# Performance work log

Hardware: AMD Instinct MI355X
Metric: run time of the kernel (lower is better)

Reference implementation:

```python
import jax, jax.numpy as jnp
import numpy as np

# geomloss SamplesLoss defaults: loss='sinkhorn', p=2, blur=0.05, scaling=0.5,
# reach=None (balanced -> dampening lambda = 1), diameter=3, debias=False.
P = 2
DIAMETER = 3.0
BLUR = 0.05
SCALING = 0.5
MARGIN = 0.1
GAMMA = 10.0
# geomloss epsilon_schedule(p, diameter, blur, scaling)
EPS_LIST = [DIAMETER ** P] \
    + [float(np.exp(e)) for e in np.arange(P * np.log(DIAMETER), P * np.log(BLUR), P * np.log(SCALING))] \
    + [BLUR ** P]
NEG_INF_LOGW = -100000.0  # geomloss log_weights() sentinel for zero weights


def similarity_cost(xa, xb, gamma=GAMMA):
    # F.normalize(x, dim=-1): x / max(||x||, 1e-12)
    xa = xa / jnp.clip(jnp.linalg.norm(xa, axis=-1, keepdims=True), 1e-12)
    xb = xb / jnp.clip(jnp.linalg.norm(xb, axis=-1, keepdims=True), 1e-12)
    sim = jnp.exp(jnp.einsum('bnd,bmd->bnm', xa, xb) * gamma)  # (B, N, M)
    sim_c = sim.sum(axis=1, keepdims=True)  # column sums (B, 1, M)
    sim_r = sim.sum(axis=2, keepdims=True)  # row sums    (B, N, 1)
    return 1.0 - sim / (sim_c + sim_r - sim)


def softmin(eps, C, h):
    # geomloss softmin_tensorized: -eps * logsumexp_j(h_j - C_ij/eps)
    # C: (B, N, M), h: (B_or_1, M) -> (B, N)
    return -eps * jax.nn.logsumexp(h[:, None, :] - C / eps, axis=2)


def sinkhorn_ot(alpha, a_log, beta, b_log, f1, f2):
    # geomloss sinkhorn_tensorized with debias=False, balanced OT.
    C_xy = similarity_cost(f1, jax.lax.stop_gradient(f2))  # cost(x, y.detach())
    C_yx = similarity_cost(f2, jax.lax.stop_gradient(f1))  # cost(y, x.detach())
    C_xy_sg = jax.lax.stop_gradient(C_xy)
    C_yx_sg = jax.lax.stop_gradient(C_yx)

    eps = EPS_LIST[0]
    g_ab = softmin(eps, C_yx_sg, a_log)  # dual potential on y
    f_ba = softmin(eps, C_xy_sg, b_log)  # dual potential on x
    for eps in EPS_LIST:
        # symmetric (averaged) Sinkhorn updates, no grad (geomloss runs under no_grad)
        ft = softmin(eps, C_xy_sg, b_log + g_ab / eps)
        gt = softmin(eps, C_yx_sg, a_log + f_ba / eps)
        f_ba, g_ab = 0.5 * (f_ba + ft), 0.5 * (g_ab + gt)

    # last extrapolation: only differentiable step (detached dual inputs)
    eps = EPS_LIST[-1]
    f_ba_new = softmin(eps, C_xy, jax.lax.stop_gradient(b_log + g_ab / eps))
    g_ab_new = softmin(eps, C_yx, jax.lax.stop_gradient(a_log + f_ba / eps))

    # sinkhorn_cost (debias=False): <alpha, f_ba> + <beta, g_ab>
    return (alpha * f_ba_new).sum(axis=1) + (beta * g_ab_new).sum(axis=1)  # (B,)


def setup_inputs() -> dict:
    key = jax.random.key(0)
    k1, k2, k3, k4, k5 = jax.random.split(key, 5)
    B, N, N1, M1, D = 16, 512, 384, 384, 256
    return {
        'x1': jax.random.normal(k1, (B, N, D), dtype=jnp.float32),
        'x2': jax.random.normal(k2, (B, N, D), dtype=jnp.float32),
        'x3': jax.random.normal(k3, (B, N1, D), dtype=jnp.float32),
        'x4': jax.random.normal(k4, (B, M1, D), dtype=jnp.float32),
        'dist': jax.random.normal(k5, (16,), dtype=jnp.float32),  # stored but unused
    }


def reference(x1, x2, x3, x4, dist):
    B, N, _ = x1.shape
    N1 = x3.shape[1]
    M1 = x4.shape[1]
    dt = x1.dtype
    # marginals: ones over real points, zeros over padding points
    alpha = jnp.concatenate([jnp.ones((1, N), dt), jnp.zeros((1, N1), dt)], axis=1)
    beta = jnp.concatenate([jnp.ones((1, N), dt), jnp.zeros((1, M1), dt)], axis=1)
    a_log = jnp.concatenate([jnp.zeros((1, N), dt), jnp.full((1, N1), NEG_INF_LOGW, dt)], axis=1)
    b_log = jnp.concatenate([jnp.zeros((1, N), dt), jnp.full((1, M1), NEG_INF_LOGW, dt)], axis=1)

    f1 = jnp.concatenate([x1, x3], axis=1)  # (B, N+N1, D)
    f2 = jnp.concatenate([x2, x4], axis=1)  # (B, N+M1, D)

    ot_loss = sinkhorn_ot(alpha, a_log, beta, b_log, f1, f2)  # (B,)
    scon_cost = jnp.mean(ot_loss)[None]  # sum(ot_loss)/B, shape (1,)

    hinge = jax.nn.relu(MARGIN - jnp.einsum('bnd,bmd->bnm', x3, x4)).sum()
    hinge_cost = hinge[None]  # shape (1,)

    # original returns {'hinge_cost': ..., 'scon_cost': ...}; pack as (2,) array
    return jnp.concatenate([hinge_cost, scon_cost])
```

## Files before the change

kernel.cpp:

```cpp
#include <hip/hip_runtime.h>
#include <cstddef>
#include <cstdint>

#define BATCH 16
#define NFULL 896
#define NREAL 512
#define NPAD  384
#define DIM   256

typedef short bf16x8 __attribute__((ext_vector_type(8)));
typedef short s16x4  __attribute__((ext_vector_type(4)));
typedef float f32x4  __attribute__((ext_vector_type(4)));
typedef int   int4v  __attribute__((ext_vector_type(4)));

static __device__ inline short f2bf(float v) {
    unsigned u = __float_as_uint(v);
    unsigned r = (u + 0x7FFFu + ((u >> 16) & 1u)) >> 16;
    return (short)r;
}
static __device__ inline float bf2f(short s) {
    return __uint_as_float(((unsigned)(unsigned short)s) << 16);
}

__global__ __launch_bounds__(256) void norm_cvt_kernel(
    const float* __restrict__ x1, const float* __restrict__ x3,
    const float* __restrict__ x2, const float* __restrict__ x4,
    short* __restrict__ A1s, short* __restrict__ B2s,
    float* __restrict__ invn1, float* __restrict__ invn2,
    float* __restrict__ n1, float* __restrict__ n2,
    float* __restrict__ zero_base, float* __restrict__ out)
{
    const int t = threadIdx.x;
    const int gid = blockIdx.x * 256 + t;
    if (gid < 2 * BATCH * NFULL) zero_base[gid] = 0.f;
    if (gid < 2) out[gid] = 0.f;

    const int w = t >> 6, lane = t & 63;
    const int rg = blockIdx.x * 4 + w;
    const int side = rg >= BATCH * NFULL;
    const int rem  = rg - (side ? BATCH * NFULL : 0);
    const int b = rem / NFULL, row = rem % NFULL;
    const float* src;
    if (!side) src = (row < NREAL) ? x1 + ((size_t)b * NREAL + row) * DIM
                                   : x3 + ((size_t)b * NPAD + (row - NREAL)) * DIM;
    else       src = (row < NREAL) ? x2 + ((size_t)b * NREAL + row) * DIM
                                   : x4 + ((size_t)b * NPAD + (row - NREAL)) * DIM;
    const f32x4 v = ((const f32x4*)src)[lane];
    float ss = v[0]*v[0] + v[1]*v[1] + v[2]*v[2] + v[3]*v[3];
    #pragma unroll
    for (int m = 1; m < 64; m <<= 1) ss += __shfl_xor(ss, m);
    const float nrm = sqrtf(ss);
    const float inv = 1.0f / fmaxf(nrm, 1e-12f);
    if (lane == 0) {
        (side ? invn2 : invn1)[b * NFULL + row] = inv;
        (side ? n2 : n1)[b * NFULL + row] = nrm;
    }
    s16x4 hi, lo;
    #pragma unroll
    for (int c = 0; c < 4; ++c) {
        const float val = v[c] * inv;
        hi[c] = f2bf(val);
        lo[c] = f2bf(val - bf2f(hi[c]));
    }
    short* dst = (side ? B2s : A1s) + ((size_t)b * NFULL + row) * 512;
    *(s16x4*)(dst + lane * 4) = hi;
    *(s16x4*)(dst + 256 + lane * 4) = lo;
}

__global__ __launch_bounds__(256) void gram_mfma_kernel(
    const short* __restrict__ A1s, const short* __restrict__ B2s,
    const float* __restrict__ n1, const float* __restrict__ n2,
    float* __restrict__ S, float* __restrict__ rowsum, float* __restrict__ colsum,
    float* __restrict__ out_hinge)
{
    const int flat = blockIdx.x;
    const int id = (flat & 7) * 98 + (flat >> 3);
    const int b  = id / 49;
    const int r49 = id % 49;
    const int by = r49 / 7, bx = r49 % 7;
    const int i0 = by * 128;
    const int j0 = bx * 128;
    __shared__ __align__(16) short As[128][72];
    __shared__ __align__(16) short Bs[128][72];
    const int t = threadIdx.x;
    const int wid = t >> 6, lane = t & 63;
    const int wr = wid >> 1, wc = wid & 1;
    const int lr = lane & 15, lg = lane >> 4;
    f32x4 acc[4][4] = {};

    const short* gA = A1s + ((size_t)b * NFULL + i0) * 512;
    const short* gB = B2s + ((size_t)b * NFULL + j0) * 512;

    for (int step = 0; step < 12; ++step) {
        const int kb   = step * 64;
        const int koff = kb & 255;
        const int aoff = (((kb >> 8) == 1) ? 256 : 0) + koff;
        const int boff = (((kb >> 8) == 2) ? 256 : 0) + koff;
        __syncthreads();
        #pragma unroll
        for (int p = 0; p < 4; ++p) {
            const int s = p * 256 + t;
            const int row = s >> 3, c = s & 7;
            *(int4v*)((char*)&As[0][0] + row * 144 + c * 16) =
                *(const int4v*)(gA + (size_t)row * 512 + aoff + c * 8);
            *(int4v*)((char*)&Bs[0][0] + row * 144 + c * 16) =
                *(const int4v*)(gB + (size_t)row * 512 + boff + c * 8);
        }
        __syncthreads();
        #pragma unroll
        for (int kk = 0; kk < 64; kk += 32) {
            bf16x8 af[4], bg[4];
            #pragma unroll
            for (int m = 0; m < 4; ++m)
                af[m] = *(const bf16x8*)((const char*)&As[0][0]
                         + (wr * 64 + m * 16 + lr) * 144 + kk * 2 + lg * 16);
            #pragma unroll
            for (int n = 0; n < 4; ++n)
                bg[n] = *(const bf16x8*)((const char*)&Bs[0][0]
                         + (wc * 64 + n * 16 + lr) * 144 + kk * 2 + lg * 16);
            #pragma unroll
            for (int m = 0; m < 4; ++m)
                #pragma unroll
                for (int n = 0; n < 4; ++n)
                    acc[m][n] = __builtin_amdgcn_mfma_f32_16x16x32_bf16(
                        af[m], bg[n], acc[m][n], 0, 0, 0);
        }
    }

    const bool storeS = (by < 4) && (bx < 4);
    const bool hingeB = (by >= 4) && (bx >= 4);
    float rp[4][4] = {};
    float cp[4] = {};
    float hp = 0.f;
    #pragma unroll
    for (int m = 0; m < 4; ++m) {
        const int row0 = i0 + wr * 64 + m * 16 + lg * 4;
        float n1v[4] = {0.f, 0.f, 0.f, 0.f};
        if (hingeB) {
            #pragma unroll
            for (int r = 0; r < 4; ++r) n1v[r] = n1[b * NFULL + row0 + r];
        }
        #pragma unroll
        for (int n = 0; n < 4; ++n) {
            const int col = j0 + wc * 64 + n * 16 + lr;
            const f32x4 f = acc[m][n];
            float cn = 0.f;
            float sv[4];
            #pragma unroll
            for (int r = 0; r < 4; ++r) {
                sv[r] = __expf(10.f * f[r]);
                rp[m][r] += sv[r];
                cn += sv[r];
            }
            cp[n] += cn;
            if (storeS) {
                #pragma unroll
                for (int r = 0; r < 4; ++r)
                    S[((size_t)b * NREAL + row0 + r) * NREAL + col] = sv[r];
            }
            if (hingeB) {
                const float nn2 = n2[b * NFULL + col];
                #pragma unroll
                for (int r = 0; r < 4; ++r)
                    hp += fmaxf(0.1f - f[r] * n1v[r] * nn2, 0.f);
            }
        }
    }
    #pragma unroll
    for (int m = 0; m < 4; ++m)
        #pragma unroll
        for (int r = 0; r < 4; ++r) {
            float v = rp[m][r];
            v += __shfl_xor(v, 1); v += __shfl_xor(v, 2);
            v += __shfl_xor(v, 4); v += __shfl_xor(v, 8);
            if (lr == 0)
                atomicAdd(&rowsum[b * NFULL + i0 + wr * 64 + m * 16 + lg * 4 + r], v);
        }
    #pragma unroll
    for (int n = 0; n < 4; ++n) {
        float v = cp[n];
        v += __shfl_xor(v, 16); v += __shfl_xor(v, 32);
        if (lg == 0)
            atomicAdd(&colsum[b * NFULL + j0 + wc * 64 + n * 16 + lr], v);
    }
    if (hingeB) {
        #pragma unroll
        for (int m = 1; m < 64; m <<= 1) hp += __shfl_xor(hp, m);
        if (lane == 0) atomicAdd(out_hinge, hp);
    }
}

__global__ __launch_bounds__(256) void norm_kernel(
    const float* __restrict__ x1, const float* __restrict__ x3,
    const float* __restrict__ x2, const float* __restrict__ x4,
    float* __restrict__ invn1, float* __restrict__ invn2)
{
    const int w = threadIdx.x >> 6, lane = threadIdx.x & 63;
    const int rg = blockIdx.x * 4 + w;
    const int side = rg / (BATCH * NFULL);
    const int rem  = rg - side * (BATCH * NFULL);
    const int b = rem / NFULL, r = rem % NFULL;
    const float* src;
    if (side == 0)
        src = (r < NREAL) ? x1 + ((size_t)b * NREAL + r) * DIM
                          : x3 + ((size_t)b * NPAD + (r - NREAL)) * DIM;
    else
        src = (r < NREAL) ? x2 + ((size_t)b * NREAL + r) * DIM
                          : x4 + ((size_t)b * NPAD + (r - NREAL)) * DIM;
    float4 v = ((const float4*)src)[lane];
    float ss = v.x*v.x + v.y*v.y + v.z*v.z + v.w*v.w;
    #pragma unroll
    for (int m = 1; m < 64; m <<= 1) ss += __shfl_xor(ss, m);
    if (lane == 0)
        (side == 0 ? invn1 : invn2)[b * NFULL + r] = 1.0f / fmaxf(sqrtf(ss), 1e-12f);
}

__global__ __launch_bounds__(256) void gram_kernel(
    const float* __restrict__ x1, const float* __restrict__ x3,
    const float* __restrict__ x2, const float* __restrict__ x4,
    const float* __restrict__ invn1, const float* __restrict__ invn2,
    float* __restrict__ S, float* __restrict__ rowsum, float* __restrict__ colsum)
{
    const int b  = blockIdx.z;
    const int i0 = blockIdx.y * 64;
    const int j0 = blockIdx.x * 64;
    __shared__ float As[64][68];
    __shared__ float Bs[64][68];
    __shared__ float rsh[64], csh[64];
    const int t = threadIdx.x;
    const int tx = t & 15, ty = t >> 4;
    if (t < 64) { rsh[t] = 0.f; csh[t] = 0.f; }
    float acc[4][4] = {};
    const int lk = t & 63, r4 = t >> 6;
    for (int kc = 0; kc < DIM; kc += 64) {
        __syncthreads();
        #pragma unroll
        for (int rr = 0; rr < 64; rr += 4) {
            const int r = rr + r4;
            const int gi = i0 + r;
            const float* pa = (gi < NREAL) ? x1 + ((size_t)b * NREAL + gi) * DIM
                                           : x3 + ((size_t)b * NPAD + (gi - NREAL)) * DIM;
            As[r][lk] = pa[kc + lk] * invn1[b * NFULL + gi];
            const int gj = j0 + r;
            const float* pb = (gj < NREAL) ? x2 + ((size_t)b * NREAL + gj) * DIM
                                           : x4 + ((size_t)b * NPAD + (gj - NREAL)) * DIM;
            Bs[r][lk] = pb[kc + lk] * invn2[b * NFULL + gj];
        }
        __syncthreads();
        #pragma unroll
        for (int k = 0; k < 64; k += 4) {
            float4 av[4], bv[4];
            #pragma unroll
            for (int u = 0; u < 4; ++u) av[u] = *(const float4*)&As[ty + 16*u][k];
            #pragma unroll
            for (int u = 0; u < 4; ++u) bv[u] = *(const float4*)&Bs[tx + 16*u][k];
            #pragma unroll
            for (int u = 0; u < 4; ++u)
                #pragma unroll
                for (int v = 0; v < 4; ++v) {
                    acc[u][v] += av[u].x * bv[v].x;
                    acc[u][v] += av[u].y * bv[v].y;
                    acc[u][v] += av[u].z * bv[v].z;
                    acc[u][v] += av[u].w * bv[v].w;
                }
        }
    }
    float rpart[4] = {}, cpart[4] = {};
    const bool store = (i0 < NREAL) && (j0 < NREAL);
    #pragma unroll
    for (int u = 0; u < 4; ++u)
        #pragma unroll
        for (int v = 0; v < 4; ++v) {
            const float s = __expf(10.0f * acc[u][v]);
            rpart[u] += s;
            cpart[v] += s;
            if (store) {
                const int i = i0 + ty + 16*u, j = j0 + tx + 16*v;
                S[((size_t)b * NREAL + i) * NREAL + j] = s;
            }
        }
    #pragma unroll
    for (int u = 0; u < 4; ++u) atomicAdd(&rsh[ty + 16*u], rpart[u]);
    #pragma unroll
    for (int v = 0; v < 4; ++v) atomicAdd(&csh[tx + 16*v], cpart[v]);
    __syncthreads();
    if (t < 64) {
        atomicAdd(&rowsum[b * NFULL + i0 + t], rsh[t]);
        atomicAdd(&colsum[b * NFULL + j0 + t], csh[t]);
    }
}

__global__ __launch_bounds__(256) void hinge_kernel(
    const float* __restrict__ x3, const float* __restrict__ x4, float* __restrict__ out)
{
    const int b  = blockIdx.z;
    const int i0 = blockIdx.y * 64;
    const int j0 = blockIdx.x * 64;
    __shared__ float As[64][68];
    __shared__ float Bs[64][68];
    const int t = threadIdx.x;
    const int tx = t & 15, ty = t >> 4;
    float acc[4][4] = {};
    const int lk = t & 63, r4 = t >> 6;
    for (int kc = 0; kc < DIM; kc += 64) {
        __syncthreads();
        #pragma unroll
        for (int rr = 0; rr < 64; rr += 4) {
            const int r = rr + r4;
            As[r][lk] = x3[((size_t)b * NPAD + i0 + r) * DIM + kc + lk];
            Bs[r][lk] = x4[((size_t)b * NPAD + j0 + r) * DIM + kc + lk];
        }
        __syncthreads();
        #pragma unroll
        for (int k = 0; k < 64; k += 4) {
            float4 av[4], bv[4];
            #pragma unroll
            for (int u = 0; u < 4; ++u) av[u] = *(const float4*)&As[ty + 16*u][k];
            #pragma unroll
            for (int u = 0; u < 4; ++u) bv[u] = *(const float4*)&Bs[tx + 16*u][k];
            #pragma unroll
            for (int u = 0; u < 4; ++u)
                #pragma unroll
                for (int v = 0; v < 4; ++v) {
                    acc[u][v] += av[u].x * bv[v].x;
                    acc[u][v] += av[u].y * bv[v].y;
                    acc[u][v] += av[u].z * bv[v].z;
                    acc[u][v] += av[u].w * bv[v].w;
                }
        }
    }
    float part = 0.f;
    #pragma unroll
    for (int u = 0; u < 4; ++u)
        #pragma unroll
        for (int v = 0; v < 4; ++v) part += fmaxf(0.1f - acc[u][v], 0.f);
    __shared__ float red[256];
    red[t] = part;
    __syncthreads();
    for (int s = 128; s > 0; s >>= 1) { if (t < s) red[t] += red[t + s]; __syncthreads(); }
    if (t == 0) atomicAdd(out, red[0]);
}

__global__ __launch_bounds__(256) void cost_kernel(
    float* __restrict__ C, float* __restrict__ CT,
    const float* __restrict__ rowsum, const float* __restrict__ colsum)
{
    const int b  = blockIdx.z;
    const int i0 = blockIdx.y * 64, j0 = blockIdx.x * 64;
    __shared__ float tile[64][65];
    const int t = threadIdx.x;
    const int lj = t & 63, r4 = t >> 6;
    #pragma unroll
    for (int rr = 0; rr < 64; rr += 4) {
        const int li = rr + r4;
        const size_t idx = ((size_t)b * NREAL + i0 + li) * NREAL + j0 + lj;
        const float s  = C[idx];
        const float rs = rowsum[b * NFULL + i0 + li];
        const float cs = colsum[b * NFULL + j0 + lj];
        const float c = 1.0f - s / (rs + cs - s);
        C[idx] = c;
        tile[li][lj] = c;
    }
    if (CT == nullptr) return;
    __syncthreads();
    #pragma unroll
    for (int rr = 0; rr < 4 * 16; rr += 4) {
        const int lc = rr + r4;
        CT[((size_t)b * NREAL + j0 + lc) * NREAL + i0 + lj] = tile[lj][lc];
    }
}

__global__ __launch_bounds__(256) void softmin_kernel(
    const float* __restrict__ C, const float* __restrict__ CT,
    const float* __restrict__ f_in, const float* __restrict__ g_in,
    float* __restrict__ f_out, float* __restrict__ g_out,
    float eps, int mode, float* __restrict__ out)
{
    const int w = threadIdx.x >> 6, lane = threadIdx.x & 63;
    const int rg = blockIdx.x * 4 + w;
    const int side = rg >= 2048;
    const int rem  = side ? rg - 2048 : rg;
    const int b  = rem >> 7;
    const int ib = (rem & 127) * 4;
    const float inv_eps = 1.0f / eps;
    const float* h_src = (side ? f_in : g_in) + b * NREAL;

    f32x4 h0 = {0.f, 0.f, 0.f, 0.f}, h1 = h0;
    if (mode != 0) {
        const f32x4* h4 = (const f32x4*)h_src;
        h0 = h4[lane] * inv_eps;
        h1 = h4[64 + lane] * inv_eps;
    }

    const float* Mb;
    size_t stride;
    if (!side)   { Mb = C  + ((size_t)(b * NREAL + ib)) * NREAL; stride = 1; }
    else if (CT) { Mb = CT + ((size_t)(b * NREAL + ib)) * NREAL; stride = 1; }
    else         { Mb = C + (size_t)b * NREAL * NREAL + ib;      stride = NREAL; }

    float res[4];
    float acc_res = 0.f;
    if (stride == 1) {
        f32x4 A0[4], A1[4];
        #pragma unroll
        for (int rr = 0; rr < 4; ++rr) {
            const f32x4* M4 = (const f32x4*)(Mb + (size_t)rr * NREAL);
            A0[rr] = M4[lane];
            A1[rr] = M4[64 + lane];
        }
        #pragma unroll
        for (int rr = 0; rr < 4; ++rr) {
            const f32x4 v0 = h0 - A0[rr] * inv_eps;
            const f32x4 v1 = h1 - A1[rr] * inv_eps;
            float mx = fmaxf(fmaxf(fmaxf(v0[0], v0[1]), fmaxf(v0[2], v0[3])),
                             fmaxf(fmaxf(v1[0], v1[1]), fmaxf(v1[2], v1[3])));
            #pragma unroll
            for (int off = 1; off < 64; off <<= 1) mx = fmaxf(mx, __shfl_xor(mx, off));
            float s = 0.f;
            #pragma unroll
            for (int c = 0; c < 4; ++c) s += __expf(v0[c] - mx);
            #pragma unroll
            for (int c = 0; c < 4; ++c) s += __expf(v1[c] - mx);
            #pragma unroll
            for (int off = 1; off < 64; off <<= 1) s += __shfl_xor(s, off);
            res[rr] = -eps * (mx + __logf(s));
            acc_res += res[rr];
        }
    } else {
        #pragma unroll
        for (int rr = 0; rr < 4; ++rr) {
            const float* M = Mb + rr;
            float v[8];
            #pragma unroll
            for (int q = 0; q < 8; ++q) {
                const float h = (q < 4) ? h0[q & 3] : h1[q & 3];
                v[q] = h - M[(size_t)((q & 3) + (q >> 2) * 256 + lane * 4) * NREAL
                             - (size_t)(lane * 4 + (q & 3) + (q >> 2) * 256) * 0] * inv_eps;
            }
            #pragma unroll
            for (int q = 0; q < 8; ++q) {
                const int j = (q >> 2) * 256 + lane * 4 + (q & 3);
                v[q] = ((q < 4) ? h0[q & 3] : h1[q & 3]) - M[(size_t)j * NREAL] * inv_eps;
            }
            float mx = v[0];
            #pragma unroll
            for (int q = 1; q < 8; ++q) mx = fmaxf(mx, v[q]);
            #pragma unroll
            for (int off = 1; off < 64; off <<= 1) mx = fmaxf(mx, __shfl_xor(mx, off));
            float s = 0.f;
            #pragma unroll
            for (int q = 0; q < 8; ++q) s += __expf(v[q] - mx);
            #pragma unroll
            for (int off = 1; off < 64; off <<= 1) s += __shfl_xor(s, off);
            res[rr] = -eps * (mx + __logf(s));
            acc_res += res[rr];
        }
    }

    if (mode == 2) {
        __shared__ float sred[4];
        if (lane == 0) sred[w] = acc_res;
        __syncthreads();
        if (threadIdx.x == 0)
            atomicAdd(out, (sred[0] + sred[1] + sred[2] + sred[3]) * (1.0f / BATCH));
    } else if (lane == 0) {
        float* st = (side ? g_out : f_out) + b * NREAL + ib;
        if (mode == 0) {
            *(f32x4*)st = f32x4{res[0], res[1], res[2], res[3]};
        } else {
            const f32x4 si = *(const f32x4*)((side ? g_in : f_in) + b * NREAL + ib);
            *(f32x4*)st = 0.5f * (si + f32x4{res[0], res[1], res[2], res[3]});
        }
    }
}

extern "C" void kernel_launch(void* const* d_in, const int* in_sizes, int n_in,
                              void* d_out, int out_size, void* d_ws, size_t ws_size,
                              hipStream_t stream)
{
    const float* x1 = (const float*)d_in[0];
    const float* x2 = (const float*)d_in[1];
    const float* x3 = (const float*)d_in[2];
    const float* x4 = (const float*)d_in[3];
    float* out = (float*)d_out;

    char* p = (char*)d_ws;
    const size_t CBYTES = (size_t)BATCH * NREAL * NREAL * 4;
    const size_t ABYTES = (size_t)BATCH * NFULL * 512 * 2;
    const size_t NB = (size_t)BATCH * NFULL * 4;
    const size_t PB = (size_t)BATCH * NREAL * 4;
    const size_t SMALLB = 6 * NB + 4 * PB;
    const bool mfma_ok = ws_size >= CBYTES + 2 * ABYTES + SMALLB;

    float* C = (float*)p; p += CBYTES;
    short* A1s = nullptr; short* B2s = nullptr;
    float* CT = nullptr;
    if (mfma_ok) {
        A1s = (short*)p; p += ABYTES;
        B2s = (short*)p; p += ABYTES;
        CT = (float*)A1s;
    }
    float* rowsum = (float*)p; p += NB;
    float* colsum = (float*)p; p += NB;
    float* invn1  = (float*)p; p += NB;
    float* invn2  = (float*)p; p += NB;
    float* n1     = (float*)p; p += NB;
    float* n2     = (float*)p; p += NB;
    float* fs     = (float*)p; p += 2 * PB;
    float* gs     = (float*)p; p += 2 * PB;
    if (!mfma_ok && ws_size >= (size_t)(p - (char*)d_ws) + CBYTES) {
        CT = (float*)p; p += CBYTES;
    }
    const int PS = BATCH * NREAL;

    if (mfma_ok) {
        norm_cvt_kernel<<<(2 * BATCH * NFULL) / 4, 256, 0, stream>>>(
            x1, x3, x2, x4, A1s, B2s, invn1, invn2, n1, n2, rowsum, out);
        gram_mfma_kernel<<<784, 256, 0, stream>>>(
            A1s, B2s, n1, n2, C, rowsum, colsum, out);
    } else {
        hipMemsetAsync(out, 0, 2 * sizeof(float), stream);
        hipMemsetAsync(rowsum, 0, 2 * NB, stream);
        norm_kernel<<<(2 * BATCH * NFULL) / 4, 256, 0, stream>>>(
            x1, x3, x2, x4, invn1, invn2);
        gram_kernel<<<dim3(14, 14, BATCH), 256, 0, stream>>>(
            x1, x3, x2, x4, invn1, invn2, C, rowsum, colsum);
        hinge_kernel<<<dim3(6, 6, BATCH), 256, 0, stream>>>(x3, x4, out);
    }
    cost_kernel<<<dim3(8, 8, BATCH), 256, 0, stream>>>(C, CT, rowsum, colsum);

    const int SMB = 1024;
    const float epsl[8] = {9.0f, 9.0f, 2.25f, 0.5625f, 0.140625f,
                           0.03515625f, 0.0087890625f, 0.0025f};

    softmin_kernel<<<SMB, 256, 0, stream>>>(C, CT, fs, gs, fs, gs, 9.0f, 0, out);
    int cur = 0;
    for (int k = 0; k < 8; ++k) {
        softmin_kernel<<<SMB, 256, 0, stream>>>(C, CT,
            fs + cur * PS, gs + cur * PS,
            fs + (1 - cur) * PS, gs + (1 - cur) * PS,
            epsl[k], 1, out);
        cur ^= 1;
    }
    softmin_kernel<<<SMB, 256, 0, stream>>>(C, CT,
        fs + cur * PS, gs + cur * PS, nullptr, nullptr,
        0.0025f, 2, out + 1);
}
```

Measured before the change: 200.8 us.

## Double-buffer gram tiles via direct global-to-LDS loads and XCD-aware block mapping

The gram MFMA kernel now stages operands with global_load_lds into double-buffered, XOR-swizzled shared tiles of 32-wide K slices, so the next slice's load overlaps the current MFMAs. This replaces register-staged copies and the full sync pair per step. Row and column sum atomics are skipped for padding tiles that are never used. The cost and softmin kernels remap block indices so each XCD handles two batches, keeping C rows in that XCD's L2. The risks are manual vmcnt counting, more barriers per K step, and a changed softmin register-prefetch pattern.

```diff
diff --git a/kernel.cpp b/kernel.cpp
--- a/kernel.cpp
+++ b/kernel.cpp
@@ -11,7 +11,6 @@
 typedef short bf16x8 __attribute__((ext_vector_type(8)));
 typedef short s16x4  __attribute__((ext_vector_type(4)));
 typedef float f32x4  __attribute__((ext_vector_type(4)));
-typedef int   int4v  __attribute__((ext_vector_type(4)));
 
 static __device__ inline short f2bf(float v) {
     unsigned u = __float_as_uint(v);
@@ -20,6 +19,15 @@
 }
 static __device__ inline float bf2f(short s) {
     return __uint_as_float(((unsigned)(unsigned short)s) << 16);
+}
+
+static __device__ __forceinline__ void gload_lds16(const void* g, size_t lds_byte_off,
+                                                   void* lds_base) {
+    __builtin_amdgcn_global_load_lds(
+        (const __attribute__((address_space(1))) unsigned int*)(size_t)g,
+        (__attribute__((address_space(3))) unsigned int*)(unsigned int)
+            ((size_t)lds_base + lds_byte_off),
+        16, 0, 0);
 }
 
 __global__ __launch_bounds__(256) void norm_cvt_kernel(
@@ -80,8 +88,8 @@
     const int by = r49 / 7, bx = r49 % 7;
     const int i0 = by * 128;
     const int j0 = bx * 128;
-    __shared__ __align__(16) short As[128][72];
-    __shared__ __align__(16) short Bs[128][72];
+    __shared__ __align__(16) short As[2][128][32];
+    __shared__ __align__(16) short Bs[2][128][32];
     const int t = threadIdx.x;
     const int wid = t >> 6, lane = t & 63;
     const int wr = wid >> 1, wc = wid & 1;
@@ -91,41 +99,64 @@
     const short* gA = A1s + ((size_t)b * NFULL + i0) * 512;
     const short* gB = B2s + ((size_t)b * NFULL + j0) * 512;
 
-    for (int step = 0; step < 12; ++step) {
-        const int kb   = step * 64;
-        const int koff = kb & 255;
-        const int aoff = (((kb >> 8) == 1) ? 256 : 0) + koff;
-        const int boff = (((kb >> 8) == 2) ? 256 : 0) + koff;
-        __syncthreads();
-        #pragma unroll
-        for (int p = 0; p < 4; ++p) {
-            const int s = p * 256 + t;
-            const int row = s >> 3, c = s & 7;
-            *(int4v*)((char*)&As[0][0] + row * 144 + c * 16) =
-                *(const int4v*)(gA + (size_t)row * 512 + aoff + c * 8);
-            *(int4v*)((char*)&Bs[0][0] + row * 144 + c * 16) =
-                *(const int4v*)(gB + (size_t)row * 512 + boff + c * 8);
-        }
-        __syncthreads();
-        #pragma unroll
-        for (int kk = 0; kk < 64; kk += 32) {
-            bf16x8 af[4], bg[4];
-            #pragma unroll
-            for (int m = 0; m < 4; ++m)
-                af[m] = *(const bf16x8*)((const char*)&As[0][0]
-                         + (wr * 64 + m * 16 + lr) * 144 + kk * 2 + lg * 16);
+    int srow[2], scl[2];
+    #pragma unroll
+    for (int p = 0; p < 2; ++p) {
+        const int s = p * 256 + t;
+        srow[p] = s >> 2;
+        scl[p] = (s & 3) ^ (srow[p] & 3);
+    }
+
+    #define GRAM_ISSUE(step, buf)                                              \
+        do {                                                                   \
+            const int kb_   = (step) * 32;                                     \
+            const int koff_ = kb_ & 255;                                       \
+            const int aoff_ = (((kb_ >> 8) == 1) ? 256 : 0) + koff_;           \
+            const int boff_ = (((kb_ >> 8) == 2) ? 256 : 0) + koff_;           \
+            _Pragma("unroll")                                                  \
+            for (int p = 0; p < 2; ++p)                                        \
+                gload_lds16(gA + (size_t)srow[p] * 512 + aoff_ + scl[p] * 8,   \
+                            (size_t)(p * 256 + wid * 64) * 16,                 \
+                            &As[buf][0][0]);                                   \
+            _Pragma("unroll")                                                  \
+            for (int p = 0; p < 2; ++p)                                        \
+                gload_lds16(gB + (size_t)srow[p] * 512 + boff_ + scl[p] * 8,   \
+                            (size_t)(p * 256 + wid * 64) * 16,                 \
+                            &Bs[buf][0][0]);                                   \
+        } while (0)
+
+    GRAM_ISSUE(0, 0);
+    for (int step = 0; step < 24; ++step) {
+        const int cur = step & 1;
+        if (step + 1 < 24) {
+            GRAM_ISSUE(step + 1, cur ^ 1);
+            asm volatile("s_waitcnt vmcnt(4)" ::: "memory");
+        } else {
+            asm volatile("s_waitcnt vmcnt(0)" ::: "memory");
+        }
+        __builtin_amdgcn_s_barrier();
+        bf16x8 af[4], bg[4];
+        #pragma unroll
+        for (int m = 0; m < 4; ++m) {
+            const int row = wr * 64 + m * 16 + lr;
+            af[m] = *(const bf16x8*)((const char*)&As[cur][0][0]
+                     + row * 64 + (((lg) ^ (row & 3)) << 4));
+        }
+        #pragma unroll
+        for (int n = 0; n < 4; ++n) {
+            const int row = wc * 64 + n * 16 + lr;
+            bg[n] = *(const bf16x8*)((const char*)&Bs[cur][0][0]
+                     + row * 64 + (((lg) ^ (row & 3)) << 4));
+        }
+        #pragma unroll
+        for (int m = 0; m < 4; ++m)
             #pragma unroll
             for (int n = 0; n < 4; ++n)
-                bg[n] = *(const bf16x8*)((const char*)&Bs[0][0]
-                         + (wc * 64 + n * 16 + lr) * 144 + kk * 2 + lg * 16);
-            #pragma unroll
-            for (int m = 0; m < 4; ++m)
-                #pragma unroll
-                for (int n = 0; n < 4; ++n)
-                    acc[m][n] = __builtin_amdgcn_mfma_f32_16x16x32_bf16(
-                        af[m], bg[n], acc[m][n], 0, 0, 0);
-        }
-    }
+                acc[m][n] = __builtin_amdgcn_mfma_f32_16x16x32_bf16(
+                    af[m], bg[n], acc[m][n], 0, 0, 0);
+        __builtin_amdgcn_s_barrier();
+    }
+    #undef GRAM_ISSUE
 
     const bool storeS = (by < 4) && (bx < 4);
     const bool hingeB = (by >= 4) && (bx >= 4);
@@ -166,27 +197,139 @@
             }
         }
     }
-    #pragma unroll
-    for (int m = 0; m < 4; ++m)
-        #pragma unroll
-        for (int r = 0; r < 4; ++r) {
-            float v = rp[m][r];
-            v += __shfl_xor(v, 1); v += __shfl_xor(v, 2);
-            v += __shfl_xor(v, 4); v += __shfl_xor(v, 8);
-            if (lr == 0)
-                atomicAdd(&rowsum[b * NFULL + i0 + wr * 64 + m * 16 + lg * 4 + r], v);
-        }
-    #pragma unroll
-    for (int n = 0; n < 4; ++n) {
-        float v = cp[n];
-        v += __shfl_xor(v, 16); v += __shfl_xor(v, 32);
-        if (lg == 0)
-            atomicAdd(&colsum[b * NFULL + j0 + wc * 64 + n * 16 + lr], v);
+    if (by < 4) {
+        #pragma unroll
+        for (int m = 0; m < 4; ++m)
+            #pragma unroll
+            for (int r = 0; r < 4; ++r) {
+                float v = rp[m][r];
+                v += __shfl_xor(v, 1); v += __shfl_xor(v, 2);
+                v += __shfl_xor(v, 4); v += __shfl_xor(v, 8);
+                if (lr == 0)
+                    atomicAdd(&rowsum[b * NFULL + i0 + wr * 64 + m * 16 + lg * 4 + r], v);
+            }
+    }
+    if (bx < 4) {
+        #pragma unroll
+        for (int n = 0; n < 4; ++n) {
+            float v = cp[n];
+            v += __shfl_xor(v, 16); v += __shfl_xor(v, 32);
+            if (lg == 0)
+                atomicAdd(&colsum[b * NFULL + j0 + wc * 64 + n * 16 + lr], v);
+        }
     }
     if (hingeB) {
         #pragma unroll
         for (int m = 1; m < 64; m <<= 1) hp += __shfl_xor(hp, m);
         if (lane == 0) atomicAdd(out_hinge, hp);
+    }
+}
+
+__global__ __launch_bounds__(256) void cost_kernel(
+    float* __restrict__ C, float* __restrict__ CT,
+    const float* __restrict__ rowsum, const float* __restrict__ colsum)
+{
+    const int blk = blockIdx.x;
+    const int xcd = blk & 7, q = blk >> 3;
+    const int b = 2 * xcd + (q >> 6);
+    const int t64 = q & 63;
+    const int i0 = (t64 >> 3) * 64, j0 = (t64 & 7) * 64;
+    __shared__ float tile[64][65];
+    const int t = threadIdx.x;
+    const int lj = t & 63, r4 = t >> 6;
+    #pragma unroll
+    for (int rr = 0; rr < 64; rr += 4) {
+        const int li = rr + r4;
+        const size_t idx = ((size_t)b * NREAL + i0 + li) * NREAL + j0 + lj;
+        const float s  = C[idx];
+        const float c = 1.0f - s / (rowsum[b * NFULL + i0 + li]
+                                    + colsum[b * NFULL + j0 + lj] - s);
+        C[idx] = c;
+        tile[li][lj] = c;
+    }
+    if (CT == nullptr) return;
+    __syncthreads();
+    #pragma unroll
+    for (int rr = 0; rr < 64; rr += 4) {
+        const int lc = rr + r4;
+        CT[((size_t)b * NREAL + j0 + lc) * NREAL + i0 + lj] = tile[lj][lc];
+    }
+}
+
+__global__ __launch_bounds__(256) void softmin_kernel(
+    const float* __restrict__ C, const float* __restrict__ CT,
+    const float* __restrict__ f_in, const float* __restrict__ g_in,
+    float* __restrict__ f_out, float* __restrict__ g_out,
+    float eps, int mode, float* __restrict__ out)
+{
+    const int w = threadIdx.x >> 6, lane = threadIdx.x & 63;
+    const int blk = blockIdx.x;
+    const int xcd = blk & 7, q = blk >> 3;
+    const int b = 2 * xcd + (q >> 6);
+    const int side = (q >> 5) & 1;
+    const int ib = ((q & 31) * 4 + w) * 4;
+    const float inv_eps = 1.0f / eps;
+    const float* h_src = (side ? f_in : g_in) + b * NREAL;
+
+    f32x4 h0 = {0.f, 0.f, 0.f, 0.f}, h1 = h0;
+    if (mode != 0) {
+        const f32x4* h4 = (const f32x4*)h_src;
+        h0 = h4[lane] * inv_eps;
+        h1 = h4[64 + lane] * inv_eps;
+    }
+    const float* Mb;
+    size_t stride;
+    if (!side)   { Mb = C  + ((size_t)(b * NREAL + ib)) * NREAL; stride = 1; }
+    else if (CT) { Mb = CT + ((size_t)(b * NREAL + ib)) * NREAL; stride = 1; }
+    else         { Mb = C + (size_t)b * NREAL * NREAL + ib;      stride = NREAL; }
+
+    float res[4];
+    float acc_res = 0.f;
+    #pragma unroll
+    for (int rr = 0; rr < 4; ++rr) {
+        float v[8];
+        if (stride == 1) {
+            const f32x4* M4 = (const f32x4*)(Mb + (size_t)rr * NREAL);
+            const f32x4 a0 = M4[lane], a1 = M4[64 + lane];
+            #pragma unroll
+            for (int c = 0; c < 4; ++c) { v[c] = h0[c] - a0[c] * inv_eps;
+                                          v[4+c] = h1[c] - a1[c] * inv_eps; }
+        } else {
+            const float* M = Mb + rr;
+            #pragma unroll
+            for (int qq = 0; qq < 8; ++qq) {
+                const int j = (qq >> 2) * 256 + lane * 4 + (qq & 3);
+                v[qq] = ((qq < 4) ? h0[qq & 3] : h1[qq & 3])
+                        - M[(size_t)j * NREAL] * inv_eps;
+            }
+        }
+        float mx = v[0];
+        #pragma unroll
+        for (int qq = 1; qq < 8; ++qq) mx = fmaxf(mx, v[qq]);
+        #pragma unroll
+        for (int off = 1; off < 64; off <<= 1) mx = fmaxf(mx, __shfl_xor(mx, off));
+        float s = 0.f;
+        #pragma unroll
+        for (int qq = 0; qq < 8; ++qq) s += __expf(v[qq] - mx);
+        #pragma unroll
+        for (int off = 1; off < 64; off <<= 1) s += __shfl_xor(s, off);
+        res[rr] = -eps * (mx + __logf(s));
+        acc_res += res[rr];
+    }
+    if (mode == 2) {
+        __shared__ float sred[4];
+        if (lane == 0) sred[w] = acc_res;
+        __syncthreads();
+        if (threadIdx.x == 0)
+            atomicAdd(out, (sred[0] + sred[1] + sred[2] + sred[3]) * (1.0f / BATCH));
+    } else if (lane == 0) {
+        float* st = (side ? g_out : f_out) + b * NREAL + ib;
+        if (mode == 0) {
+            *(f32x4*)st = f32x4{res[0], res[1], res[2], res[3]};
+        } else {
+            const f32x4 si = *(const f32x4*)((side ? g_in : f_in) + b * NREAL + ib);
+            *(f32x4*)st = 0.5f * (si + f32x4{res[0], res[1], res[2], res[3]});
+        }
     }
 }
 
@@ -341,139 +484,6 @@
     if (t == 0) atomicAdd(out, red[0]);
 }
 
-__global__ __launch_bounds__(256) void cost_kernel(
-    float* __restrict__ C, float* __restrict__ CT,
-    const float* __restrict__ rowsum, const float* __restrict__ colsum)
-{
-    const int b  = blockIdx.z;
-    const int i0 = blockIdx.y * 64, j0 = blockIdx.x * 64;
-    __shared__ float tile[64][65];
-    const int t = threadIdx.x;
-    const int lj = t & 63, r4 = t >> 6;
-    #pragma unroll
-    for (int rr = 0; rr < 64; rr += 4) {
-        const int li = rr + r4;
-        const size_t idx = ((size_t)b * NREAL + i0 + li) * NREAL + j0 + lj;
-        const float s  = C[idx];
-        const float rs = rowsum[b * NFULL + i0 + li];
-        const float cs = colsum[b * NFULL + j0 + lj];
-        const float c = 1.0f - s / (rs + cs - s);
-        C[idx] = c;
-        tile[li][lj] = c;
-    }
-    if (CT == nullptr) return;
-    __syncthreads();
-    #pragma unroll
-    for (int rr = 0; rr < 4 * 16; rr += 4) {
-        const int lc = rr + r4;
-        CT[((size_t)b * NREAL + j0 + lc) * NREAL + i0 + lj] = tile[lj][lc];
-    }
-}
-
-__global__ __launch_bounds__(256) void softmin_kernel(
-    const float* __restrict__ C, const float* __restrict__ CT,
-    const float* __restrict__ f_in, const float* __restrict__ g_in,
-    float* __restrict__ f_out, float* __restrict__ g_out,
-    float eps, int mode, float* __restrict__ out)
-{
-    const int w = threadIdx.x >> 6, lane = threadIdx.x & 63;
-    const int rg = blockIdx.x * 4 + w;
-    const int side = rg >= 2048;
-    const int rem  = side ? rg - 2048 : rg;
-    const int b  = rem >> 7;
-    const int ib = (rem & 127) * 4;
-    const float inv_eps = 1.0f / eps;
-    const float* h_src = (side ? f_in : g_in) + b * NREAL;
-
-    f32x4 h0 = {0.f, 0.f, 0.f, 0.f}, h1 = h0;
-    if (mode != 0) {
-        const f32x4* h4 = (const f32x4*)h_src;
-        h0 = h4[lane] * inv_eps;
-        h1 = h4[64 + lane] * inv_eps;
-    }
-
-    const float* Mb;
-    size_t stride;
-    if (!side)   { Mb = C  + ((size_t)(b * NREAL + ib)) * NREAL; stride = 1; }
-    else if (CT) { Mb = CT + ((size_t)(b * NREAL + ib)) * NREAL; stride = 1; }
-    else         { Mb = C + (size_t)b * NREAL * NREAL + ib;      stride = NREAL; }
-
-    float res[4];
-    float acc_res = 0.f;
-    if (stride == 1) {
-        f32x4 A0[4], A1[4];
-        #pragma unroll
-        for (int rr = 0; rr < 4; ++rr) {
-            const f32x4* M4 = (const f32x4*)(Mb + (size_t)rr * NREAL);
-            A0[rr] = M4[lane];
-            A1[rr] = M4[64 + lane];
-        }
-        #pragma unroll
-        for (int rr = 0; rr < 4; ++rr) {
-            const f32x4 v0 = h0 - A0[rr] * inv_eps;
-            const f32x4 v1 = h1 - A1[rr] * inv_eps;
-            float mx = fmaxf(fmaxf(fmaxf(v0[0], v0[1]), fmaxf(v0[2], v0[3])),
-                             fmaxf(fmaxf(v1[0], v1[1]), fmaxf(v1[2], v1[3])));
-            #pragma unroll
-            for (int off = 1; off < 64; off <<= 1) mx = fmaxf(mx, __shfl_xor(mx, off));
-            float s = 0.f;
-            #pragma unroll
-            for (int c = 0; c < 4; ++c) s += __expf(v0[c] - mx);
-            #pragma unroll
-            for (int c = 0; c < 4; ++c) s += __expf(v1[c] - mx);
-            #pragma unroll
-            for (int off = 1; off < 64; off <<= 1) s += __shfl_xor(s, off);
-            res[rr] = -eps * (mx + __logf(s));
-            acc_res += res[rr];
-        }
-    } else {
-        #pragma unroll
-        for (int rr = 0; rr < 4; ++rr) {
-            const float* M = Mb + rr;
-            float v[8];
-            #pragma unroll
-            for (int q = 0; q < 8; ++q) {
-                const float h = (q < 4) ? h0[q & 3] : h1[q & 3];
-                v[q] = h - M[(size_t)((q & 3) + (q >> 2) * 256 + lane * 4) * NREAL
-                             - (size_t)(lane * 4 + (q & 3) + (q >> 2) * 256) * 0] * inv_eps;
-            }
-            #pragma unroll
-            for (int q = 0; q < 8; ++q) {
-                const int j = (q >> 2) * 256 + lane * 4 + (q & 3);
-                v[q] = ((q < 4) ? h0[q & 3] : h1[q & 3]) - M[(size_t)j * NREAL] * inv_eps;
-            }
-            float mx = v[0];
-            #pragma unroll
-            for (int q = 1; q < 8; ++q) mx = fmaxf(mx, v[q]);
-            #pragma unroll
-            for (int off = 1; off < 64; off <<= 1) mx = fmaxf(mx, __shfl_xor(mx, off));
-            float s = 0.f;
-            #pragma unroll
-            for (int q = 0; q < 8; ++q) s += __expf(v[q] - mx);
-            #pragma unroll
-            for (int off = 1; off < 64; off <<= 1) s += __shfl_xor(s, off);
-            res[rr] = -eps * (mx + __logf(s));
-            acc_res += res[rr];
-        }
-    }
-
-    if (mode == 2) {
-        __shared__ float sred[4];
-        if (lane == 0) sred[w] = acc_res;
-        __syncthreads();
-        if (threadIdx.x == 0)
-            atomicAdd(out, (sred[0] + sred[1] + sred[2] + sred[3]) * (1.0f / BATCH));
-    } else if (lane == 0) {
-        float* st = (side ? g_out : f_out) + b * NREAL + ib;
-        if (mode == 0) {
-            *(f32x4*)st = f32x4{res[0], res[1], res[2], res[3]};
-        } else {
-            const f32x4 si = *(const f32x4*)((side ? g_in : f_in) + b * NREAL + ib);
-            *(f32x4*)st = 0.5f * (si + f32x4{res[0], res[1], res[2], res[3]});
-        }
-    }
-}
-
 extern "C" void kernel_launch(void* const* d_in, const int* in_sizes, int n_in,
                               void* d_out, int out_size, void* d_ws, size_t ws_size,
                               hipStream_t stream)
@@ -527,22 +537,21 @@
             x1, x3, x2, x4, invn1, invn2, C, rowsum, colsum);
         hinge_kernel<<<dim3(6, 6, BATCH), 256, 0, stream>>>(x3, x4, out);
     }
-    cost_kernel<<<dim3(8, 8, BATCH), 256, 0, stream>>>(C, CT, rowsum, colsum);
-
-    const int SMB = 1024;
+
+    cost_kernel<<<1024, 256, 0, stream>>>(C, CT, rowsum, colsum);
+
     const float epsl[8] = {9.0f, 9.0f, 2.25f, 0.5625f, 0.140625f,
                            0.03515625f, 0.0087890625f, 0.0025f};
-
-    softmin_kernel<<<SMB, 256, 0, stream>>>(C, CT, fs, gs, fs, gs, 9.0f, 0, out);
+    softmin_kernel<<<1024, 256, 0, stream>>>(C, CT, fs, gs, fs, gs, 9.0f, 0, out);
     int cur = 0;
     for (int k = 0; k < 8; ++k) {
-        softmin_kernel<<<SMB, 256, 0, stream>>>(C, CT,
+        softmin_kernel<<<1024, 256, 0, stream>>>(C, CT,
             fs + cur * PS, gs + cur * PS,
             fs + (1 - cur) * PS, gs + (1 - cur) * PS,
             epsl[k], 1, out);
         cur ^= 1;
     }
-    softmin_kernel<<<SMB, 256, 0, stream>>>(C, CT,
+    softmin_kernel<<<1024, 256, 0, stream>>>(C, CT,
         fs + cur * PS, gs + cur * PS, nullptr, nullptr,
         0.0025f, 2, out + 1);
 }
```

New measurement: 201.8 us. Within noise of the previous version (+0.5%).
